# Optimization experiments

Hardware: AMD Instinct MI355X
Metric: run time of the kernel (lower is better)

The kernel has to match this reference:

```python
import jax, jax.numpy as jnp
import numpy as np

ALPHA, BETA, GAMMA = 0.5, 0.003, 0.001
NUM_CLASSES = 1000
NUM_FEATURES = 1000
BATCH = 16384


def setup_inputs() -> dict:
    key = jax.random.key(0)
    k1, k2, k3 = jax.random.split(key, 3)
    x = jax.random.normal(k1, (BATCH, NUM_FEATURES), dtype=jnp.float32)
    y = jax.random.randint(k2, (BATCH,), 0, NUM_CLASSES)
    centers = jax.random.normal(k3, (NUM_CLASSES, NUM_FEATURES), dtype=jnp.float32)
    return {"x": x, "y": y, "centers": centers}


def reference(x, y, centers):
    B = x.shape[0]
    C = NUM_CLASSES
    # cross entropy (x used as logits, as in nn.CrossEntropyLoss)
    logp = jax.nn.log_softmax(x, axis=-1)
    ce = -jnp.mean(jnp.take_along_axis(logp, y[:, None], axis=1))
    # center loss on PRE-update centers
    c_y = centers[y]                       # [B, F]
    delta = x - c_y
    center_loss = jnp.mean(jnp.sum(delta * delta, axis=1))
    # functional form of the in-place per-class center update:
    # centers[i] += alpha * mean(delta[y == i])
    counts = jax.ops.segment_sum(jnp.ones((B,), x.dtype), y, num_segments=C)  # [C]
    sum_delta = jax.ops.segment_sum(delta, y, num_segments=C)                 # [C, F]
    mean_delta = jnp.where(counts[:, None] > 0,
                           sum_delta / jnp.maximum(counts, 1)[:, None],
                           jnp.zeros_like(sum_delta))
    new_centers = centers + ALPHA * mean_delta
    # inter loss: sum_{i<j} ||c_i - c_j||^2 = C*sum_i||c_i||^2 - ||sum_i c_i||^2
    sq = jnp.sum(new_centers * new_centers, axis=1)   # [C]
    s = jnp.sum(new_centers, axis=0)                  # [F]
    num_pairs = C * (C - 1) / 2
    inter_loss = (C * jnp.sum(sq) - jnp.sum(s * s)) / num_pairs
    # intra loss on POST-update centers: mean over class, averaged over classes
    d2 = jnp.sum((x - new_centers[y]) ** 2, axis=1)   # [B]
    per_class_sum = jax.ops.segment_sum(d2, y, num_segments=C)
    per_class_mean = jnp.where(counts > 0, per_class_sum / jnp.maximum(counts, 1),
                               jnp.zeros_like(per_class_sum))
    intra_loss = jnp.sum(per_class_mean) / C
    return ce + BETA * center_loss + GAMMA * inter_loss + GAMMA * intra_loss
```

## Files before the change

kernel.cpp:

```cpp
#include <hip/hip_runtime.h>
#include <math.h>

#define NF 1000
#define NC 1000
#define NB 16384
#define NV 250
#define ALPHA_C 0.5f
#define BETA_C 0.003f
#define GAMMA_C 0.001f
#define MAXL 512
#define NCHUNK 16
#define NFB 4

__device__ __forceinline__ float wave_sum(float v) {
#pragma unroll
    for (int off = 32; off > 0; off >>= 1) v += __shfl_xor(v, off, 64);
    return v;
}
__device__ __forceinline__ float wave_max(float v) {
#pragma unroll
    for (int off = 32; off > 0; off >>= 1) v = fmaxf(v, __shfl_xor(v, off, 64));
    return v;
}

__global__ __launch_bounds__(256) void class_fused(
    const float* __restrict__ x, const int* __restrict__ y,
    const float* __restrict__ centers,
    float* __restrict__ new_centers, float4* __restrict__ partials,
    int* __restrict__ done_cnt) {
    __shared__ int list[MAXL];
    __shared__ int lcount;
    __shared__ float4 smx[NV];
    __shared__ float sb[8];
    const int c = blockIdx.x, t = threadIdx.x;
    const int wid = t >> 6, lane = t & 63;
    if (c == 0 && t == 0) *done_cnt = 0;
    if (t == 0) lcount = 0;
    __syncthreads();

    const int4* y4 = (const int4*)y;
    for (int i = t; i < NB / 4; i += 256) {
        int4 v = y4[i];
        int b = 4 * i;
        if (v.x == c) { int p = atomicAdd(&lcount, 1); list[p & (MAXL - 1)] = b; }
        if (v.y == c) { int p = atomicAdd(&lcount, 1); list[p & (MAXL - 1)] = b + 1; }
        if (v.z == c) { int p = atomicAdd(&lcount, 1); list[p & (MAXL - 1)] = b + 2; }
        if (v.w == c) { int p = atomicAdd(&lcount, 1); list[p & (MAXL - 1)] = b + 3; }
    }
    __syncthreads();
    const int n = lcount;

    const float4* crow = (const float4*)(centers + (size_t)c * NF);
    const bool tail = (lane < NV - 192);
    const float4 z4 = make_float4(0.f, 0.f, 0.f, 0.f);
    const float4 c0 = crow[lane];
    const float4 c1 = crow[lane + 64];
    const float4 c2 = crow[lane + 128];
    const float4 c3 = tail ? crow[lane + 192] : z4;

    const int f4 = c >> 2;
    const int j_src = f4 >> 6, lane_src = f4 & 63, comp = c & 3;

    float4 a0 = z4, a1 = z4, a2 = z4, a3 = z4;
    float ce_acc = 0.f, s2_acc = 0.f;

    const float NEG = -INFINITY;
    const float4 ninf4 = make_float4(NEG, NEG, NEG, NEG);

    float4 v0 = ninf4, v1 = ninf4, v2 = ninf4, v3 = ninf4;
    if (wid < n) {
        const float4* r = (const float4*)(x + (size_t)list[wid] * NF);
        v0 = r[lane]; v1 = r[lane + 64]; v2 = r[lane + 128];
        v3 = tail ? r[lane + 192] : ninf4;
    }

    for (int i = wid; i < n; i += 4) {
        const int inx = i + 4;
        float4 n0 = ninf4, n1 = ninf4, n2 = ninf4, n3 = ninf4;
        if (inx < n) {
            const float4* r = (const float4*)(x + (size_t)list[inx] * NF);
            n0 = r[lane]; n1 = r[lane + 64]; n2 = r[lane + 128];
            n3 = tail ? r[lane + 192] : ninf4;
        }

        float m = fmaxf(fmaxf(v0.x, v0.y), fmaxf(v0.z, v0.w));
        m = fmaxf(m, fmaxf(fmaxf(v1.x, v1.y), fmaxf(v1.z, v1.w)));
        m = fmaxf(m, fmaxf(fmaxf(v2.x, v2.y), fmaxf(v2.z, v2.w)));
        m = fmaxf(m, fmaxf(fmaxf(v3.x, v3.y), fmaxf(v3.z, v3.w)));
        const float rmax = wave_max(m);

        float e = expf(v0.x - rmax) + expf(v0.y - rmax) +
                  expf(v0.z - rmax) + expf(v0.w - rmax);
        e += expf(v1.x - rmax) + expf(v1.y - rmax) +
             expf(v1.z - rmax) + expf(v1.w - rmax);
        e += expf(v2.x - rmax) + expf(v2.y - rmax) +
             expf(v2.z - rmax) + expf(v2.w - rmax);
        e += expf(v3.x - rmax) + expf(v3.y - rmax) +
             expf(v3.z - rmax) + expf(v3.w - rmax);

        float d;
        {
            float dx = v0.x - c0.x, dy = v0.y - c0.y, dz = v0.z - c0.z, dw = v0.w - c0.w;
            d = dx * dx + dy * dy + dz * dz + dw * dw;
            a0.x += v0.x; a0.y += v0.y; a0.z += v0.z; a0.w += v0.w;
        }
        {
            float dx = v1.x - c1.x, dy = v1.y - c1.y, dz = v1.z - c1.z, dw = v1.w - c1.w;
            d += dx * dx + dy * dy + dz * dz + dw * dw;
            a1.x += v1.x; a1.y += v1.y; a1.z += v1.z; a1.w += v1.w;
        }
        {
            float dx = v2.x - c2.x, dy = v2.y - c2.y, dz = v2.z - c2.z, dw = v2.w - c2.w;
            d += dx * dx + dy * dy + dz * dz + dw * dw;
            a2.x += v2.x; a2.y += v2.y; a2.z += v2.z; a2.w += v2.w;
        }
        if (tail) {
            float dx = v3.x - c3.x, dy = v3.y - c3.y, dz = v3.z - c3.z, dw = v3.w - c3.w;
            d += dx * dx + dy * dy + dz * dz + dw * dw;
            a3.x += v3.x; a3.y += v3.y; a3.z += v3.z; a3.w += v3.w;
        }
        const float se = wave_sum(e);
        const float sd = wave_sum(d);

        float4 xj = (j_src == 0) ? v0 : (j_src == 1) ? v1 : (j_src == 2) ? v2 : v3;
        float cand = (comp == 0) ? xj.x : (comp == 1) ? xj.y : (comp == 2) ? xj.z : xj.w;
        const float xy = __shfl(cand, lane_src, 64);

        ce_acc += -(xy - rmax - logf(se));
        s2_acc += sd;

        v0 = n0; v1 = n1; v2 = n2; v3 = n3;
    }

    for (int w = 0; w < 4; w++) {
        if (wid == w) {
            if (w == 0) {
                smx[lane] = a0; smx[lane + 64] = a1; smx[lane + 128] = a2;
                if (tail) smx[lane + 192] = a3;
            } else {
                float4 s;
                s = smx[lane];      s.x += a0.x; s.y += a0.y; s.z += a0.z; s.w += a0.w; smx[lane] = s;
                s = smx[lane + 64]; s.x += a1.x; s.y += a1.y; s.z += a1.z; s.w += a1.w; smx[lane + 64] = s;
                s = smx[lane + 128]; s.x += a2.x; s.y += a2.y; s.z += a2.z; s.w += a2.w; smx[lane + 128] = s;
                if (tail) { s = smx[lane + 192]; s.x += a3.x; s.y += a3.y; s.z += a3.z; s.w += a3.w; smx[lane + 192] = s; }
            }
        }
        __syncthreads();
    }
    if (lane == 0) { sb[wid] = ce_acc; sb[4 + wid] = s2_acc; }
    __syncthreads();

    if (wid == 0) {
        const float inv = (n > 0) ? 1.f / (float)n : 0.f;
        const float has = (n > 0) ? 1.f : 0.f;
        float lsq = 0.f, lmd2 = 0.f;
        float4* ncrow = (float4*)(new_centers + (size_t)c * NF);
#pragma unroll
        for (int j = 0; j < 4; j++) {
            const int idx = lane + 64 * j;
            if (idx < NV) {
                const float4 s = smx[idx];
                const float4 cv = (j == 0) ? c0 : (j == 1) ? c1 : (j == 2) ? c2 : c3;
                float4 md, nc;
                md.x = has * (s.x * inv - cv.x);
                md.y = has * (s.y * inv - cv.y);
                md.z = has * (s.z * inv - cv.z);
                md.w = has * (s.w * inv - cv.w);
                nc.x = cv.x + ALPHA_C * md.x; nc.y = cv.y + ALPHA_C * md.y;
                nc.z = cv.z + ALPHA_C * md.z; nc.w = cv.w + ALPHA_C * md.w;
                ncrow[idx] = nc;
                lsq  += nc.x * nc.x + nc.y * nc.y + nc.z * nc.z + nc.w * nc.w;
                lmd2 += md.x * md.x + md.y * md.y + md.z * md.z + md.w * md.w;
            }
        }
        const float sq = wave_sum(lsq);
        const float md2 = wave_sum(lmd2);
        if (lane == 0) {
            const float ces = sb[0] + sb[1] + sb[2] + sb[3];
            const float s2 = sb[4] + sb[5] + sb[6] + sb[7];
            const float intra = (n > 0) ? (s2 * inv - ALPHA_C * (2.f - ALPHA_C) * md2) : 0.f;
            partials[c] = make_float4(ces, s2, sq, intra);
        }
    }
}

__global__ __launch_bounds__(256) void col_finalize(
    const float* __restrict__ new_centers, const float4* __restrict__ partials,
    float* __restrict__ s_part, int* __restrict__ done_cnt,
    float* __restrict__ out) {
    const int t = threadIdx.x;
    const int f = blockIdx.x * 256 + t;
    if (f < NF) {
        float acc = 0.f;
        for (int c = blockIdx.y; c < NC; c += NCHUNK)
            acc += new_centers[(size_t)c * NF + f];
        s_part[blockIdx.y * NF + f] = acc;
    }
    __threadfence();
    __shared__ int s_last;
    __syncthreads();
    if (t == 0) s_last = atomicAdd(done_cnt, 1);
    __syncthreads();
    if (s_last != NFB * NCHUNK - 1) return;

    __shared__ float sb[80];
    float ssq = 0.f, ces = 0.f, s2 = 0.f, sq = 0.f, intra = 0.f;
    for (int col = t; col < NC; col += 256) {
        float s = 0.f;
#pragma unroll
        for (int k = 0; k < NCHUNK; k++) s += s_part[k * NF + col];
        ssq += s * s;
        float4 p = partials[col];
        ces += p.x; s2 += p.y; sq += p.z; intra += p.w;
    }
    float w0 = wave_sum(ssq), w1 = wave_sum(ces), w2 = wave_sum(s2);
    float w3 = wave_sum(sq), w4 = wave_sum(intra);
    const int wid = t >> 6, lane = t & 63;
    if (lane == 0) {
        sb[wid] = w0; sb[16 + wid] = w1; sb[32 + wid] = w2;
        sb[48 + wid] = w3; sb[64 + wid] = w4;
    }
    __syncthreads();
    if (t == 0) {
        float Sssq = 0.f, Sces = 0.f, Ss2 = 0.f, Ssq = 0.f, Sintra = 0.f;
        for (int k = 0; k < 4; k++) {
            Sssq += sb[k]; Sces += sb[16 + k]; Ss2 += sb[32 + k];
            Ssq += sb[48 + k]; Sintra += sb[64 + k];
        }
        float cem = Sces / (float)NB;
        float cl = Ss2 / (float)NB;
        float num_pairs = (float)NC * (float)(NC - 1) * 0.5f;
        float inter = ((float)NC * Ssq - Sssq) / num_pairs;
        float intra_l = Sintra / (float)NC;
        out[0] = cem + BETA_C * cl + GAMMA_C * inter + GAMMA_C * intra_l;
    }
}

extern "C" void kernel_launch(void* const* d_in, const int* in_sizes, int n_in,
                              void* d_out, int out_size, void* d_ws, size_t ws_size,
                              hipStream_t stream) {
    const float* x = (const float*)d_in[0];
    const int* y = (const int*)d_in[1];
    const float* centers = (const float*)d_in[2];
    float* out = (float*)d_out;

    char* ws = (char*)d_ws;
    float* s_part      = (float*)(ws);
    float4* partials   = (float4*)(ws + 64000);
    int* done_cnt      = (int*)(ws + 80000);
    float* new_centers = (float*)(ws + 80064);

    class_fused<<<NC, 256, 0, stream>>>(x, y, centers, new_centers, partials,
                                        done_cnt);
    dim3 cgrid(NFB, NCHUNK);
    col_finalize<<<cgrid, 256, 0, stream>>>(new_centers, partials, s_part,
                                            done_cnt, out);
}
```

Baseline: 142.9 us.

## Use 8 waves per class block with parallel shared-memory reduction and fast exp/log

```diff
diff --git a/kernel.cpp b/kernel.cpp
--- a/kernel.cpp
+++ b/kernel.cpp
@@ -11,6 +11,7 @@
 #define MAXL 512
 #define NCHUNK 16
 #define NFB 4
+#define WAVES 8
 
 __device__ __forceinline__ float wave_sum(float v) {
 #pragma unroll
@@ -23,15 +24,15 @@
     return v;
 }
 
-__global__ __launch_bounds__(256) void class_fused(
+__global__ __launch_bounds__(512) void class_fused(
     const float* __restrict__ x, const int* __restrict__ y,
     const float* __restrict__ centers,
     float* __restrict__ new_centers, float4* __restrict__ partials,
     int* __restrict__ done_cnt) {
     __shared__ int list[MAXL];
     __shared__ int lcount;
-    __shared__ float4 smx[NV];
-    __shared__ float sb[8];
+    __shared__ float4 smx8[WAVES][NV];
+    __shared__ float sb_ce[WAVES], sb_s2[WAVES], sb_lsq[WAVES], sb_md2[WAVES];
     const int c = blockIdx.x, t = threadIdx.x;
     const int wid = t >> 6, lane = t & 63;
     if (c == 0 && t == 0) *done_cnt = 0;
@@ -39,7 +40,8 @@
     __syncthreads();
 
     const int4* y4 = (const int4*)y;
-    for (int i = t; i < NB / 4; i += 256) {
+#pragma unroll
+    for (int i = t; i < NB / 4; i += 512) {
         int4 v = y4[i];
         int b = 4 * i;
         if (v.x == c) { int p = atomicAdd(&lcount, 1); list[p & (MAXL - 1)] = b; }
@@ -74,8 +76,8 @@
         v3 = tail ? r[lane + 192] : ninf4;
     }
 
-    for (int i = wid; i < n; i += 4) {
-        const int inx = i + 4;
+    for (int i = wid; i < n; i += WAVES) {
+        const int inx = i + WAVES;
         float4 n0 = ninf4, n1 = ninf4, n2 = ninf4, n3 = ninf4;
         if (inx < n) {
             const float4* r = (const float4*)(x + (size_t)list[inx] * NF);
@@ -89,14 +91,14 @@
         m = fmaxf(m, fmaxf(fmaxf(v3.x, v3.y), fmaxf(v3.z, v3.w)));
         const float rmax = wave_max(m);
 
-        float e = expf(v0.x - rmax) + expf(v0.y - rmax) +
-                  expf(v0.z - rmax) + expf(v0.w - rmax);
-        e += expf(v1.x - rmax) + expf(v1.y - rmax) +
-             expf(v1.z - rmax) + expf(v1.w - rmax);
-        e += expf(v2.x - rmax) + expf(v2.y - rmax) +
-             expf(v2.z - rmax) + expf(v2.w - rmax);
-        e += expf(v3.x - rmax) + expf(v3.y - rmax) +
-             expf(v3.z - rmax) + expf(v3.w - rmax);
+        float e = __expf(v0.x - rmax) + __expf(v0.y - rmax) +
+                  __expf(v0.z - rmax) + __expf(v0.w - rmax);
+        e += __expf(v1.x - rmax) + __expf(v1.y - rmax) +
+             __expf(v1.z - rmax) + __expf(v1.w - rmax);
+        e += __expf(v2.x - rmax) + __expf(v2.y - rmax) +
+             __expf(v2.z - rmax) + __expf(v2.w - rmax);
+        e += __expf(v3.x - rmax) + __expf(v3.y - rmax) +
+             __expf(v3.z - rmax) + __expf(v3.w - rmax);
 
         float d;
         {
@@ -126,61 +128,54 @@
         float cand = (comp == 0) ? xj.x : (comp == 1) ? xj.y : (comp == 2) ? xj.z : xj.w;
         const float xy = __shfl(cand, lane_src, 64);
 
-        ce_acc += -(xy - rmax - logf(se));
+        ce_acc += -(xy - rmax - __logf(se));
         s2_acc += sd;
 
         v0 = n0; v1 = n1; v2 = n2; v3 = n3;
     }
 
-    for (int w = 0; w < 4; w++) {
-        if (wid == w) {
-            if (w == 0) {
-                smx[lane] = a0; smx[lane + 64] = a1; smx[lane + 128] = a2;
-                if (tail) smx[lane + 192] = a3;
-            } else {
-                float4 s;
-                s = smx[lane];      s.x += a0.x; s.y += a0.y; s.z += a0.z; s.w += a0.w; smx[lane] = s;
-                s = smx[lane + 64]; s.x += a1.x; s.y += a1.y; s.z += a1.z; s.w += a1.w; smx[lane + 64] = s;
-                s = smx[lane + 128]; s.x += a2.x; s.y += a2.y; s.z += a2.z; s.w += a2.w; smx[lane + 128] = s;
-                if (tail) { s = smx[lane + 192]; s.x += a3.x; s.y += a3.y; s.z += a3.z; s.w += a3.w; smx[lane + 192] = s; }
-            }
-        }
-        __syncthreads();
-    }
-    if (lane == 0) { sb[wid] = ce_acc; sb[4 + wid] = s2_acc; }
-    __syncthreads();
-
-    if (wid == 0) {
-        const float inv = (n > 0) ? 1.f / (float)n : 0.f;
-        const float has = (n > 0) ? 1.f : 0.f;
-        float lsq = 0.f, lmd2 = 0.f;
-        float4* ncrow = (float4*)(new_centers + (size_t)c * NF);
-#pragma unroll
-        for (int j = 0; j < 4; j++) {
-            const int idx = lane + 64 * j;
-            if (idx < NV) {
-                const float4 s = smx[idx];
-                const float4 cv = (j == 0) ? c0 : (j == 1) ? c1 : (j == 2) ? c2 : c3;
-                float4 md, nc;
-                md.x = has * (s.x * inv - cv.x);
-                md.y = has * (s.y * inv - cv.y);
-                md.z = has * (s.z * inv - cv.z);
-                md.w = has * (s.w * inv - cv.w);
-                nc.x = cv.x + ALPHA_C * md.x; nc.y = cv.y + ALPHA_C * md.y;
-                nc.z = cv.z + ALPHA_C * md.z; nc.w = cv.w + ALPHA_C * md.w;
-                ncrow[idx] = nc;
-                lsq  += nc.x * nc.x + nc.y * nc.y + nc.z * nc.z + nc.w * nc.w;
-                lmd2 += md.x * md.x + md.y * md.y + md.z * md.z + md.w * md.w;
-            }
-        }
-        const float sq = wave_sum(lsq);
-        const float md2 = wave_sum(lmd2);
-        if (lane == 0) {
-            const float ces = sb[0] + sb[1] + sb[2] + sb[3];
-            const float s2 = sb[4] + sb[5] + sb[6] + sb[7];
-            const float intra = (n > 0) ? (s2 * inv - ALPHA_C * (2.f - ALPHA_C) * md2) : 0.f;
-            partials[c] = make_float4(ces, s2, sq, intra);
-        }
+    smx8[wid][lane] = a0;
+    smx8[wid][lane + 64] = a1;
+    smx8[wid][lane + 128] = a2;
+    if (tail) smx8[wid][lane + 192] = a3;
+    if (lane == 0) { sb_ce[wid] = ce_acc; sb_s2[wid] = s2_acc; }
+    __syncthreads();
+
+    float lsq = 0.f, lmd2 = 0.f;
+    const float inv = (n > 0) ? 1.f / (float)n : 0.f;
+    const float has = (n > 0) ? 1.f : 0.f;
+    if (t < NV) {
+        float4 s = smx8[0][t];
+#pragma unroll
+        for (int w = 1; w < WAVES; w++) {
+            float4 p = smx8[w][t];
+            s.x += p.x; s.y += p.y; s.z += p.z; s.w += p.w;
+        }
+        const float4 cv = crow[t];
+        float4 md, nc;
+        md.x = has * (s.x * inv - cv.x);
+        md.y = has * (s.y * inv - cv.y);
+        md.z = has * (s.z * inv - cv.z);
+        md.w = has * (s.w * inv - cv.w);
+        nc.x = cv.x + ALPHA_C * md.x; nc.y = cv.y + ALPHA_C * md.y;
+        nc.z = cv.z + ALPHA_C * md.z; nc.w = cv.w + ALPHA_C * md.w;
+        ((float4*)(new_centers + (size_t)c * NF))[t] = nc;
+        lsq  = nc.x * nc.x + nc.y * nc.y + nc.z * nc.z + nc.w * nc.w;
+        lmd2 = md.x * md.x + md.y * md.y + md.z * md.z + md.w * md.w;
+    }
+    lsq = wave_sum(lsq);
+    lmd2 = wave_sum(lmd2);
+    if (lane == 0) { sb_lsq[wid] = lsq; sb_md2[wid] = lmd2; }
+    __syncthreads();
+    if (t == 0) {
+        float sq = 0.f, md2 = 0.f, ces = 0.f, s2 = 0.f;
+#pragma unroll
+        for (int w = 0; w < WAVES; w++) {
+            sq += sb_lsq[w]; md2 += sb_md2[w];
+            ces += sb_ce[w]; s2 += sb_s2[w];
+        }
+        const float intra = (n > 0) ? (s2 * inv - ALPHA_C * (2.f - ALPHA_C) * md2) : 0.f;
+        partials[c] = make_float4(ces, s2, sq, intra);
     }
 }
 
@@ -250,7 +245,7 @@
     int* done_cnt      = (int*)(ws + 80000);
     float* new_centers = (float*)(ws + 80064);
 
-    class_fused<<<NC, 256, 0, stream>>>(x, y, centers, new_centers, partials,
+    class_fused<<<NC, 512, 0, stream>>>(x, y, centers, new_centers, partials,
                                         done_cnt);
     dim3 cgrid(NFB, NCHUNK);
     col_finalize<<<cgrid, 256, 0, stream>>>(new_centers, partials, s_part,
```

Result: no change. 142.2 us (-0.5%).
